# Kernel tuning notes

Measured on AMD Instinct MI355X. Metric: run time of the kernel, lower is better.

## Reference

```python
import jax, jax.numpy as jnp
import numpy as np

NB_NEIGHBORS = 8


def _euclidean_distances(X):
    # X: (n, d); pairwise distances between rows, clamped at 0 before sqrt.
    sq = jnp.sum(jnp.square(X), axis=1)  # (n,)
    d = -2.0 * (X @ X.T) + sq[None, :] + sq[:, None]
    return jnp.sqrt(jnp.maximum(d, 0.0))


def setup_inputs() -> dict:
    key = jax.random.key(0)
    k1, k2 = jax.random.split(key)
    B, C, F, D3 = 64, 4, 8192, 1
    d_coord = 64
    inputs = jax.random.normal(k1, (B, C, F, D3), dtype=jnp.float32)
    coordinates = jax.random.normal(k2, (d_coord, 1, F), dtype=jnp.float32)
    return {"inputs": inputs, "coordinates": coordinates}


def reference(inputs, coordinates):
    # coordinates: (d, 1, F) -> crd: (d, F); features are columns.
    d, _, F = coordinates.shape
    crd = coordinates.reshape(d, F)
    dist = _euclidean_distances(crd.T)  # (F, F) distances between features
    # top-k smallest distances per feature (indices of nearest features)
    _, idx = jax.lax.top_k(-dist, NB_NEIGHBORS)  # (F, K)
    # Original loop: first slot hardcoded to feature 0, then idx[0,1:],
    # then idx[f,:] for f >= 1. Flatten into one gather index vector.
    flat_idx = jnp.concatenate(
        [jnp.zeros((1,), dtype=idx.dtype), idx[0, 1:], idx[1:].reshape(-1)]
    )  # (F*K,)
    # Single fused gather along the feature axis: (B, C, F*K, D3)
    return jnp.take(inputs, flat_idx, axis=2)
```

## Files before the change

kernel.cpp:

```cpp
#include <hip/hip_runtime.h>

#define F      8192
#define KD     64
#define NB     8
#define WROWS  32
#define MKEEP  16
#define JQ     4
#define CPR    64
#define NROUND ((F / JQ) / CPR)
#define CAP    96
#define MARGIN 0.25f

typedef unsigned long long u64;
typedef unsigned short ushort_t;
typedef __attribute__((ext_vector_type(8))) _Float16 f16x8;
typedef __attribute__((ext_vector_type(4))) float f32x4;

__device__ __forceinline__ u64 pack64(float d, int j) {
    return ((u64)__float_as_uint(d) << 32) | (unsigned)j;
}

template<int CTRL>
__device__ __forceinline__ u64 dpp_u64(u64 x) {
    unsigned lo = (unsigned)x, hi = (unsigned)(x >> 32);
    lo = (unsigned)__builtin_amdgcn_update_dpp(0, (int)lo, CTRL, 0xF, 0xF, true);
    hi = (unsigned)__builtin_amdgcn_update_dpp(0, (int)hi, CTRL, 0xF, 0xF, true);
    return ((u64)hi << 32) | lo;
}
__device__ __forceinline__ u64 swap_xor1(u64 x) { return dpp_u64<0xB1>(x); }
__device__ __forceinline__ u64 swap_xor2(u64 x) { return dpp_u64<0x4E>(x); }
__device__ __forceinline__ u64 swap_xor4(u64 x, int n) {
    u64 shr = dpp_u64<0x114>(x);
    u64 shl = dpp_u64<0x104>(x);
    return (n & 4) ? shr : shl;
}
__device__ __forceinline__ u64 swap_xor8(u64 x, int n) {
    u64 shr = dpp_u64<0x118>(x);
    u64 shl = dpp_u64<0x108>(x);
    return (n & 8) ? shr : shl;
}
__device__ __forceinline__ u64 swap_mirror(u64 x) { return dpp_u64<0x140>(x); }
__device__ __forceinline__ u64 swz_xor16(u64 x) {
    unsigned lo = (unsigned)__builtin_amdgcn_ds_swizzle((int)(unsigned)x, 0x401F);
    unsigned hi = (unsigned)__builtin_amdgcn_ds_swizzle((int)(x >> 32), 0x401F);
    return ((u64)hi << 32) | lo;
}

#define CEK(x, J, K, SW)                                                      \
    { u64 px = SW; bool wmin = ((n & (J)) == 0) == ((n & (K)) == 0);          \
      x = (wmin == (px < x)) ? px : x; }
#define CEA(L, J, SW)                                                         \
    { u64 pl = SW; bool wmin = ((n & (J)) == 0);                              \
      L = (wmin == (pl < L)) ? pl : L; }
#define SORT16(x)                                                             \
    CEK(x, 1, 2,  swap_xor1(x))                                               \
    CEK(x, 2, 4,  swap_xor2(x))    CEK(x, 1, 4,  swap_xor1(x))                \
    CEK(x, 4, 8,  swap_xor4(x,n))  CEK(x, 2, 8,  swap_xor2(x))                \
    CEK(x, 1, 8,  swap_xor1(x))                                               \
    CEK(x, 8, 16, swap_xor8(x,n))  CEK(x, 4, 16, swap_xor4(x,n))              \
    CEK(x, 2, 16, swap_xor2(x))    CEK(x, 1, 16, swap_xor1(x))
#define MERGECLEAN(x, Y)                                                      \
    { u64 y = (Y); x = (y < x) ? y : x;                                       \
      CEA(x, 8, swap_xor8(x, n))                                              \
      CEA(x, 4, swap_xor4(x, n))                                              \
      CEA(x, 2, swap_xor2(x))                                                 \
      CEA(x, 1, swap_xor1(x)) }

__global__ __launch_bounds__(256) void prep_kernel(const float* __restrict__ crd,
                                                   float* __restrict__ sq,
                                                   ushort_t* __restrict__ XtH,
                                                   float* __restrict__ Xt32) {
    const int f = blockIdx.x * 256 + threadIdx.x;
    float acc = 0.f;
#pragma unroll
    for (int kb = 0; kb < 8; ++kb) {
        ushort_t hb[8];
        float    xv[8];
#pragma unroll
        for (int u = 0; u < 8; ++u) {
            int k = kb * 8 + u;
            float x = crd[k * F + f];
            acc = fmaf(x, x, acc);
            hb[u] = __builtin_bit_cast(ushort_t, (_Float16)x);
            xv[u] = x;
        }
        *(uint4*)&XtH[(size_t)f * KD + kb * 8] = *(const uint4*)hb;
        *(float4*)&Xt32[(size_t)f * KD + kb * 8]     = *(const float4*)&xv[0];
        *(float4*)&Xt32[(size_t)f * KD + kb * 8 + 4] = *(const float4*)&xv[4];
    }
    sq[f] = acc;
}

__global__ __launch_bounds__(256, 4) void knn_mfma(const ushort_t* __restrict__ XtH,
                                                   const float* __restrict__ sq,
                                                   u64* __restrict__ part) {
    __shared__ u64 buf[WROWS][CAP + 1];
    __shared__ u64 lst[WROWS][MKEEP + 1];
    __shared__ __align__(16) float thr[WROWS];
    __shared__ int cnt[WROWS];

    const int tid  = threadIdx.x;
    const int wave = tid >> 6;
    const int tx   = tid & 63;
    const int quad = tx >> 4;
    const int n    = tx & 15;
    const int blockRow = (blockIdx.x >> 2) * WROWS;
    const int jq    = blockIdx.x & 3;
    const int jbase = jq * (F / JQ);

    if (tid < WROWS) { cnt[tid] = 0; thr[tid] = __int_as_float(0x7f800000); }
#pragma unroll
    for (int e = tid; e < WROWS * MKEEP; e += 256) lst[e >> 4][e & 15] = ~0ULL;
    __syncthreads();

    const size_t a0 = (size_t)(blockRow + n) * KD + quad * 8;
    const size_t a1 = (size_t)(blockRow + 16 + n) * KD + quad * 8;
    const f16x8 a0h0 = *(const f16x8*)(XtH + a0), a0h1 = *(const f16x8*)(XtH + a0 + 32);
    const f16x8 a1h0 = *(const f16x8*)(XtH + a1), a1h1 = *(const f16x8*)(XtH + a1 + 32);
    const f32x4 sqi0 = *(const f32x4*)&sq[blockRow + quad * 4];
    const f32x4 sqi1 = *(const f32x4*)&sq[blockRow + 16 + quad * 4];
    f32x4 pre0, pre1;
#pragma unroll
    for (int r = 0; r < 4; ++r) { pre0[r] = -__int_as_float(0x7f800000);
                                  pre1[r] = -__int_as_float(0x7f800000); }

    const int laneCol = wave * 16 + n;

#define LOADB(H0, H1, SJ, RND)                                                \
    {   int jc = jbase + (RND) * CPR + laneCol;                               \
        size_t bo = (size_t)jc * KD + quad * 8;                               \
        H0 = *(const f16x8*)(XtH + bo); H1 = *(const f16x8*)(XtH + bo + 32);  \
        SJ = sq[jc]; }

#define MFMABODY(H0, H1)                                                      \
        f32x4 za0 = {0,0,0,0}, za1 = {0,0,0,0};                               \
        za0 = __builtin_amdgcn_mfma_f32_16x16x32_f16(a0h0, H0, za0, 0, 0, 0); \
        za0 = __builtin_amdgcn_mfma_f32_16x16x32_f16(a0h1, H1, za0, 0, 0, 0); \
        za1 = __builtin_amdgcn_mfma_f32_16x16x32_f16(a1h0, H0, za1, 0, 0, 0); \
        za1 = __builtin_amdgcn_mfma_f32_16x16x32_f16(a1h1, H1, za1, 0, 0, 0);

#define PROCESS0(H0, H1, SJ, RND)                                             \
    {   MFMABODY(H0, H1)                                                      \
        const int jc = jbase + (RND) * CPR + laneCol;                         \
        _Pragma("unroll")                                                     \
        for (int r = 0; r < 4; ++r) {                                         \
            float d0 = fmaxf((sqi0[r] + SJ) - 2.f * za0[r], 0.f);             \
            buf[quad * 4 + r][laneCol] = pack64(d0, jc);                      \
            float d1 = fmaxf((sqi1[r] + SJ) - 2.f * za1[r], 0.f);             \
            buf[16 + quad * 4 + r][laneCol] = pack64(d1, jc);                 \
        } }

#define PROCESS(H0, H1, SJ, RND)                                              \
    {   MFMABODY(H0, H1)                                                      \
        const int jc = jbase + (RND) * CPR + laneCol;                         \
        const float h = 0.5f * SJ;                                            \
        _Pragma("unroll")                                                     \
        for (int r = 0; r < 4; ++r) {                                         \
            float dot = za0[r];                                               \
            if (dot >= pre0[r] + h) {                                         \
                float d = fmaxf((sqi0[r] + SJ) - 2.f * dot, 0.f);             \
                int row = quad * 4 + r;                                       \
                int q = atomicAdd(&cnt[row], 1);                              \
                if (q < CAP) buf[row][q] = pack64(d, jc);                     \
            }                                                                 \
            dot = za1[r];                                                     \
            if (dot >= pre1[r] + h) {                                         \
                float d = fmaxf((sqi1[r] + SJ) - 2.f * dot, 0.f);             \
                int row = 16 + quad * 4 + r;                                  \
                int q = atomicAdd(&cnt[row], 1);                              \
                if (q < CAP) buf[row][q] = pack64(d, jc);                     \
            }                                                                 \
        } }

#define FOLD(R0)                                                              \
    {   __syncthreads();                                                      \
        _Pragma("unroll")                                                     \
        for (int p = 0; p < 2; ++p) {                                         \
            const int row = p * 16 + wave * 4 + quad;                         \
            u64 Lv = lst[row][n];                                             \
            const u64 tmax = __shfl(Lv, (tx & 48) | 15, 64);                  \
            const int nn = (R0) ? CPR : min(cnt[row], CAP);                   \
            for (int ii = 0; ii < nn; ii += 16) {                             \
                u64 x = (ii + n < nn) ? buf[row][ii + n] : ~0ULL;             \
                u64 bal = __ballot(x < tmax);                                 \
                if ((unsigned short)(bal >> (quad * 16)) == 0) continue;      \
                SORT16(x)                                                     \
                MERGECLEAN(Lv, swap_mirror(x))                                \
            }                                                                 \
            lst[row][n] = Lv;                                                 \
            if (n == NB - 1) thr[row] = __uint_as_float((unsigned)(Lv >> 32)) + MARGIN; \
            if (n == 0) cnt[row] = 0;                                         \
        }                                                                     \
        __syncthreads();                                                      \
        {   f32x4 t0 = *(const f32x4*)&thr[quad * 4];                         \
            f32x4 t1 = *(const f32x4*)&thr[16 + quad * 4];                    \
            _Pragma("unroll")                                                 \
            for (int r = 0; r < 4; ++r) {                                     \
                pre0[r] = 0.5f * (sqi0[r] - t0[r]);                           \
                pre1[r] = 0.5f * (sqi1[r] - t1[r]);                           \
            } } }

    f16x8 B0h0, B0h1, B1h0, B1h1;
    float B0sj, B1sj;
    LOADB(B0h0, B0h1, B0sj, 0)
    LOADB(B1h0, B1h1, B1sj, 1)

    PROCESS0(B0h0, B0h1, B0sj, 0)
    LOADB(B0h0, B0h1, B0sj, 2)
    FOLD(1)
    PROCESS(B1h0, B1h1, B1sj, 1)
    LOADB(B1h0, B1h1, B1sj, 3)
    FOLD(0)

    for (int rr = 2; rr < NROUND; rr += 2) {
        PROCESS(B0h0, B0h1, B0sj, rr)
        if (rr + 2 < NROUND) LOADB(B0h0, B0h1, B0sj, rr + 2)
        PROCESS(B1h0, B1h1, B1sj, rr + 1)
        if (rr + 3 < NROUND) LOADB(B1h0, B1h1, B1sj, rr + 3)
        if (((rr + 1) & (rr + 2)) == 0) FOLD(0)
    }

#pragma unroll
    for (int e = tid; e < WROWS * MKEEP; e += 256) {
        int rrw = e >> 4, ss = e & 15;
        part[((size_t)jq * F + blockRow + rrw) * MKEEP + ss] = lst[rrw][ss];
    }
#undef LOADB
#undef MFMABODY
#undef PROCESS0
#undef PROCESS
#undef FOLD
}

__global__ __launch_bounds__(256) void recheck_kernel(const float* __restrict__ Xt32,
                                                      const float* __restrict__ sq,
                                                      const u64* __restrict__ part,
                                                      int* __restrict__ knn) {
    __shared__ float A_s[4][KD];
    const int tid = threadIdx.x;
    const int rl = tid >> 6, tx = tid & 63;
    const int n  = tx & 15;
    const int i = blockIdx.x * 4 + rl;

    A_s[tid >> 6][tid & 63] = Xt32[(size_t)(blockIdx.x * 4 + (tid >> 6)) * KD + (tid & 63)];
    __syncthreads();

    u64 pc = part[((size_t)(tx >> 4) * F + i) * MKEEP + (tx & 15)];
    int j = (int)(pc & 0xffffffffu);

    const float4* b4 = (const float4*)(Xt32 + (size_t)j * KD);
    float acc = 0.f;
#pragma unroll
    for (int kk = 0; kk < KD / 4; ++kk) {
        float4 b = b4[kk];
        const float* a = &A_s[rl][kk * 4];
        acc = fmaf(a[0], b.x, acc);
        acc = fmaf(a[1], b.y, acc);
        acc = fmaf(a[2], b.z, acc);
        acc = fmaf(a[3], b.w, acc);
    }
    float d = fmaxf((sq[i] + sq[j]) - 2.f * acc, 0.f);
    u64 x = pack64(d, j);

    SORT16(x)
    MERGECLEAN(x, swz_xor16(swap_mirror(x)))
    MERGECLEAN(x, __shfl_xor(swap_mirror(x), 32, 64))

    if (tx < NB) knn[(size_t)i * NB + tx] = (int)(x & 0xffffffffu);
}

__global__ __launch_bounds__(512) void gather_kernel(const float* __restrict__ inp,
                                                     const int* __restrict__ knn,
                                                     float* __restrict__ out) {
    __shared__ float row[F];
    const int bc    = blockIdx.x >> 2;
    const int chunk = blockIdx.x & 3;
    const int tid   = threadIdx.x;

    const float4* in4  = (const float4*)(inp + (size_t)bc * F);
    float4*       row4 = (float4*)row;
#pragma unroll
    for (int i = 0; i < (F / 4) / 512; ++i) row4[i * 512 + tid] = in4[i * 512 + tid];
    __syncthreads();

    const int4* kn4 = (const int4*)knn;
    float4*     ou4 = (float4*)(out + (size_t)bc * (F * NB));

#pragma unroll
    for (int i = 0; i < 8; ++i) {
        int e = chunk * 4096 + i * 512 + tid;
        int4 idx = kn4[e];
        if (e == 0) idx.x = 0;
        float4 o;
        o.x = row[idx.x]; o.y = row[idx.y]; o.z = row[idx.z]; o.w = row[idx.w];
        ou4[e] = o;
    }
}

extern "C" void kernel_launch(void* const* d_in, const int* in_sizes, int n_in,
                              void* d_out, int out_size, void* d_ws, size_t ws_size,
                              hipStream_t stream) {
    const float* inp = (const float*)d_in[0];
    const float* crd = (const float*)d_in[1];
    float* out = (float*)d_out;

    ushort_t* XtH  = (ushort_t*)d_ws;
    float*    Xt32 = (float*)((char*)d_ws + (2u << 20));
    float*    sq   = (float*)((char*)d_ws + (4u << 20));
    int*      knn  = (int*)((char*)d_ws + (4u << 20) + (1u << 15));
    u64*      part = (u64*)((char*)d_ws + (5u << 20));

    prep_kernel<<<F / 256, 256, 0, stream>>>(crd, sq, XtH, Xt32);
    knn_mfma<<<(F / WROWS) * JQ, 256, 0, stream>>>(XtH, sq, part);
    recheck_kernel<<<F / 4, 256, 0, stream>>>(Xt32, sq, part, knn);
    gather_kernel<<<256 * 4, 512, 0, stream>>>(inp, knn, out);
}
```

Baseline: 163.2 us.

## Fuse four kernels into one persistent kernel with software grid barriers

Merges the prep, kNN MFMA, recheck and gather kernels into one 1024-block kernel whose phases are separated by atomic-counter grid barriers, with a shared-memory union reused across phases. The aim is to remove the per-launch gaps and tail drain between the four launches. In exchange it adds barrier spin and atomic traffic and relies on all 1024 blocks being resident at once, which the launch bounds suggest but do not guarantee. The gather phase now runs with 256 threads per block instead of 512, and a memset is added before each launch to reset the barrier counters.

```diff
diff --git a/kernel.cpp b/kernel.cpp
--- a/kernel.cpp
+++ b/kernel.cpp
@@ -10,6 +10,7 @@
 #define NROUND ((F / JQ) / CPR)
 #define CAP    96
 #define MARGIN 0.25f
+#define GRID   1024
 
 typedef unsigned long long u64;
 typedef unsigned short ushort_t;
@@ -18,6 +19,21 @@
 
 __device__ __forceinline__ u64 pack64(float d, int j) {
     return ((u64)__float_as_uint(d) << 32) | (unsigned)j;
+}
+
+__device__ __forceinline__ void gbar(unsigned* cnt, unsigned* rel) {
+    __syncthreads();
+    if (threadIdx.x == 0) {
+        __threadfence();
+        unsigned v = atomicAdd(cnt, 1u);
+        if (v == GRID - 1) {
+            atomicExch(rel, 1u);
+        } else {
+            while (atomicAdd(rel, 0u) == 0u) __builtin_amdgcn_s_sleep(8);
+        }
+        __threadfence();
+    }
+    __syncthreads();
 }
 
 template<int CTRL>
@@ -66,65 +82,75 @@
       CEA(x, 2, swap_xor2(x))                                                 \
       CEA(x, 1, swap_xor1(x)) }
 
-__global__ __launch_bounds__(256) void prep_kernel(const float* __restrict__ crd,
-                                                   float* __restrict__ sq,
-                                                   ushort_t* __restrict__ XtH,
-                                                   float* __restrict__ Xt32) {
-    const int f = blockIdx.x * 256 + threadIdx.x;
-    float acc = 0.f;
-#pragma unroll
-    for (int kb = 0; kb < 8; ++kb) {
-        ushort_t hb[8];
-        float    xv[8];
-#pragma unroll
-        for (int u = 0; u < 8; ++u) {
-            int k = kb * 8 + u;
-            float x = crd[k * F + f];
-            acc = fmaf(x, x, acc);
-            hb[u] = __builtin_bit_cast(ushort_t, (_Float16)x);
-            xv[u] = x;
-        }
-        *(uint4*)&XtH[(size_t)f * KD + kb * 8] = *(const uint4*)hb;
-        *(float4*)&Xt32[(size_t)f * KD + kb * 8]     = *(const float4*)&xv[0];
-        *(float4*)&Xt32[(size_t)f * KD + kb * 8 + 4] = *(const float4*)&xv[4];
-    }
-    sq[f] = acc;
-}
-
-__global__ __launch_bounds__(256, 4) void knn_mfma(const ushort_t* __restrict__ XtH,
-                                                   const float* __restrict__ sq,
-                                                   u64* __restrict__ part) {
-    __shared__ u64 buf[WROWS][CAP + 1];
-    __shared__ u64 lst[WROWS][MKEEP + 1];
-    __shared__ __align__(16) float thr[WROWS];
-    __shared__ int cnt[WROWS];
-
+__global__ __launch_bounds__(256, 4) void fused_kernel(
+        const float* __restrict__ inp, const float* __restrict__ crd,
+        float* __restrict__ out, ushort_t* __restrict__ XtH,
+        float* __restrict__ Xt32, float* __restrict__ sq,
+        int* __restrict__ knn, u64* __restrict__ part,
+        unsigned* __restrict__ bar) {
+    __shared__ union ShMem {
+        struct {
+            u64 buf[WROWS][CAP + 1];
+            u64 lst[WROWS][MKEEP + 1];
+            float thr[WROWS];
+            int cnt[WROWS];
+        } k;
+        float row[F];
+        float A_s[4][KD];
+    } sh;
+
+    const int bid  = blockIdx.x;
     const int tid  = threadIdx.x;
     const int wave = tid >> 6;
     const int tx   = tid & 63;
     const int quad = tx >> 4;
     const int n    = tx & 15;
-    const int blockRow = (blockIdx.x >> 2) * WROWS;
-    const int jq    = blockIdx.x & 3;
-    const int jbase = jq * (F / JQ);
-
-    if (tid < WROWS) { cnt[tid] = 0; thr[tid] = __int_as_float(0x7f800000); }
-#pragma unroll
-    for (int e = tid; e < WROWS * MKEEP; e += 256) lst[e >> 4][e & 15] = ~0ULL;
-    __syncthreads();
-
-    const size_t a0 = (size_t)(blockRow + n) * KD + quad * 8;
-    const size_t a1 = (size_t)(blockRow + 16 + n) * KD + quad * 8;
-    const f16x8 a0h0 = *(const f16x8*)(XtH + a0), a0h1 = *(const f16x8*)(XtH + a0 + 32);
-    const f16x8 a1h0 = *(const f16x8*)(XtH + a1), a1h1 = *(const f16x8*)(XtH + a1 + 32);
-    const f32x4 sqi0 = *(const f32x4*)&sq[blockRow + quad * 4];
-    const f32x4 sqi1 = *(const f32x4*)&sq[blockRow + 16 + quad * 4];
-    f32x4 pre0, pre1;
-#pragma unroll
-    for (int r = 0; r < 4; ++r) { pre0[r] = -__int_as_float(0x7f800000);
-                                  pre1[r] = -__int_as_float(0x7f800000); }
-
-    const int laneCol = wave * 16 + n;
+
+    if (bid < F / 256) {
+        const int f = bid * 256 + tid;
+        float acc = 0.f;
+#pragma unroll
+        for (int kb = 0; kb < 8; ++kb) {
+            ushort_t hb[8];
+            float    xv[8];
+#pragma unroll
+            for (int u = 0; u < 8; ++u) {
+                int k = kb * 8 + u;
+                float x = crd[k * F + f];
+                acc = fmaf(x, x, acc);
+                hb[u] = __builtin_bit_cast(ushort_t, (_Float16)x);
+                xv[u] = x;
+            }
+            *(uint4*)&XtH[(size_t)f * KD + kb * 8] = *(const uint4*)hb;
+            *(float4*)&Xt32[(size_t)f * KD + kb * 8]     = *(const float4*)&xv[0];
+            *(float4*)&Xt32[(size_t)f * KD + kb * 8 + 4] = *(const float4*)&xv[4];
+        }
+        sq[f] = acc;
+    }
+    gbar(&bar[0], &bar[1]);
+
+    {
+        const int blockRow = (bid >> 2) * WROWS;
+        const int jq    = bid & 3;
+        const int jbase = jq * (F / JQ);
+
+        if (tid < WROWS) { sh.k.cnt[tid] = 0; sh.k.thr[tid] = __int_as_float(0x7f800000); }
+#pragma unroll
+        for (int e = tid; e < WROWS * MKEEP; e += 256) sh.k.lst[e >> 4][e & 15] = ~0ULL;
+        __syncthreads();
+
+        const size_t a0 = (size_t)(blockRow + n) * KD + quad * 8;
+        const size_t a1 = (size_t)(blockRow + 16 + n) * KD + quad * 8;
+        const f16x8 a0h0 = *(const f16x8*)(XtH + a0), a0h1 = *(const f16x8*)(XtH + a0 + 32);
+        const f16x8 a1h0 = *(const f16x8*)(XtH + a1), a1h1 = *(const f16x8*)(XtH + a1 + 32);
+        const f32x4 sqi0 = *(const f32x4*)&sq[blockRow + quad * 4];
+        const f32x4 sqi1 = *(const f32x4*)&sq[blockRow + 16 + quad * 4];
+        f32x4 pre0, pre1;
+#pragma unroll
+        for (int r = 0; r < 4; ++r) { pre0[r] = -__int_as_float(0x7f800000);
+                                      pre1[r] = -__int_as_float(0x7f800000); }
+
+        const int laneCol = wave * 16 + n;
 
 #define LOADB(H0, H1, SJ, RND)                                                \
     {   int jc = jbase + (RND) * CPR + laneCol;                               \
@@ -145,9 +171,9 @@
         _Pragma("unroll")                                                     \
         for (int r = 0; r < 4; ++r) {                                         \
             float d0 = fmaxf((sqi0[r] + SJ) - 2.f * za0[r], 0.f);             \
-            buf[quad * 4 + r][laneCol] = pack64(d0, jc);                      \
+            sh.k.buf[quad * 4 + r][laneCol] = pack64(d0, jc);                 \
             float d1 = fmaxf((sqi1[r] + SJ) - 2.f * za1[r], 0.f);             \
-            buf[16 + quad * 4 + r][laneCol] = pack64(d1, jc);                 \
+            sh.k.buf[16 + quad * 4 + r][laneCol] = pack64(d1, jc);            \
         } }
 
 #define PROCESS(H0, H1, SJ, RND)                                              \
@@ -160,15 +186,15 @@
             if (dot >= pre0[r] + h) {                                         \
                 float d = fmaxf((sqi0[r] + SJ) - 2.f * dot, 0.f);             \
                 int row = quad * 4 + r;                                       \
-                int q = atomicAdd(&cnt[row], 1);                              \
-                if (q < CAP) buf[row][q] = pack64(d, jc);                     \
+                int q = atomicAdd(&sh.k.cnt[row], 1);                         \
+                if (q < CAP) sh.k.buf[row][q] = pack64(d, jc);                \
             }                                                                 \
             dot = za1[r];                                                     \
             if (dot >= pre1[r] + h) {                                         \
                 float d = fmaxf((sqi1[r] + SJ) - 2.f * dot, 0.f);             \
                 int row = 16 + quad * 4 + r;                                  \
-                int q = atomicAdd(&cnt[row], 1);                              \
-                if (q < CAP) buf[row][q] = pack64(d, jc);                     \
+                int q = atomicAdd(&sh.k.cnt[row], 1);                         \
+                if (q < CAP) sh.k.buf[row][q] = pack64(d, jc);                \
             }                                                                 \
         } }
 
@@ -177,123 +203,118 @@
         _Pragma("unroll")                                                     \
         for (int p = 0; p < 2; ++p) {                                         \
             const int row = p * 16 + wave * 4 + quad;                         \
-            u64 Lv = lst[row][n];                                             \
+            u64 Lv = sh.k.lst[row][n];                                        \
             const u64 tmax = __shfl(Lv, (tx & 48) | 15, 64);                  \
-            const int nn = (R0) ? CPR : min(cnt[row], CAP);                   \
+            const int nn = (R0) ? CPR : min(sh.k.cnt[row], CAP);              \
             for (int ii = 0; ii < nn; ii += 16) {                             \
-                u64 x = (ii + n < nn) ? buf[row][ii + n] : ~0ULL;             \
+                u64 x = (ii + n < nn) ? sh.k.buf[row][ii + n] : ~0ULL;        \
                 u64 bal = __ballot(x < tmax);                                 \
                 if ((unsigned short)(bal >> (quad * 16)) == 0) continue;      \
                 SORT16(x)                                                     \
                 MERGECLEAN(Lv, swap_mirror(x))                                \
             }                                                                 \
-            lst[row][n] = Lv;                                                 \
-            if (n == NB - 1) thr[row] = __uint_as_float((unsigned)(Lv >> 32)) + MARGIN; \
-            if (n == 0) cnt[row] = 0;                                         \
+            sh.k.lst[row][n] = Lv;                                            \
+            if (n == NB - 1) sh.k.thr[row] = __uint_as_float((unsigned)(Lv >> 32)) + MARGIN; \
+            if (n == 0) sh.k.cnt[row] = 0;                                    \
         }                                                                     \
         __syncthreads();                                                      \
-        {   f32x4 t0 = *(const f32x4*)&thr[quad * 4];                         \
-            f32x4 t1 = *(const f32x4*)&thr[16 + quad * 4];                    \
+        {   f32x4 t0 = *(const f32x4*)&sh.k.thr[quad * 4];                    \
+            f32x4 t1 = *(const f32x4*)&sh.k.thr[16 + quad * 4];               \
             _Pragma("unroll")                                                 \
             for (int r = 0; r < 4; ++r) {                                     \
                 pre0[r] = 0.5f * (sqi0[r] - t0[r]);                           \
                 pre1[r] = 0.5f * (sqi1[r] - t1[r]);                           \
             } } }
 
-    f16x8 B0h0, B0h1, B1h0, B1h1;
-    float B0sj, B1sj;
-    LOADB(B0h0, B0h1, B0sj, 0)
-    LOADB(B1h0, B1h1, B1sj, 1)
-
-    PROCESS0(B0h0, B0h1, B0sj, 0)
-    LOADB(B0h0, B0h1, B0sj, 2)
-    FOLD(1)
-    PROCESS(B1h0, B1h1, B1sj, 1)
-    LOADB(B1h0, B1h1, B1sj, 3)
-    FOLD(0)
-
-    for (int rr = 2; rr < NROUND; rr += 2) {
-        PROCESS(B0h0, B0h1, B0sj, rr)
-        if (rr + 2 < NROUND) LOADB(B0h0, B0h1, B0sj, rr + 2)
-        PROCESS(B1h0, B1h1, B1sj, rr + 1)
-        if (rr + 3 < NROUND) LOADB(B1h0, B1h1, B1sj, rr + 3)
-        if (((rr + 1) & (rr + 2)) == 0) FOLD(0)
-    }
-
-#pragma unroll
-    for (int e = tid; e < WROWS * MKEEP; e += 256) {
-        int rrw = e >> 4, ss = e & 15;
-        part[((size_t)jq * F + blockRow + rrw) * MKEEP + ss] = lst[rrw][ss];
-    }
+        f16x8 B0h0, B0h1, B1h0, B1h1;
+        float B0sj, B1sj;
+        LOADB(B0h0, B0h1, B0sj, 0)
+        LOADB(B1h0, B1h1, B1sj, 1)
+
+        PROCESS0(B0h0, B0h1, B0sj, 0)
+        LOADB(B0h0, B0h1, B0sj, 2)
+        FOLD(1)
+        PROCESS(B1h0, B1h1, B1sj, 1)
+        LOADB(B1h0, B1h1, B1sj, 3)
+        FOLD(0)
+
+        for (int rr = 2; rr < NROUND; rr += 2) {
+            PROCESS(B0h0, B0h1, B0sj, rr)
+            if (rr + 2 < NROUND) LOADB(B0h0, B0h1, B0sj, rr + 2)
+            PROCESS(B1h0, B1h1, B1sj, rr + 1)
+            if (rr + 3 < NROUND) LOADB(B1h0, B1h1, B1sj, rr + 3)
+            if (((rr + 1) & (rr + 2)) == 0) FOLD(0)
+        }
+
+#pragma unroll
+        for (int e = tid; e < WROWS * MKEEP; e += 256) {
+            int rrw = e >> 4, ss = e & 15;
+            part[((size_t)jq * F + blockRow + rrw) * MKEEP + ss] = sh.k.lst[rrw][ss];
+        }
 #undef LOADB
 #undef MFMABODY
 #undef PROCESS0
 #undef PROCESS
 #undef FOLD
-}
-
-__global__ __launch_bounds__(256) void recheck_kernel(const float* __restrict__ Xt32,
-                                                      const float* __restrict__ sq,
-                                                      const u64* __restrict__ part,
-                                                      int* __restrict__ knn) {
-    __shared__ float A_s[4][KD];
-    const int tid = threadIdx.x;
-    const int rl = tid >> 6, tx = tid & 63;
-    const int n  = tx & 15;
-    const int i = blockIdx.x * 4 + rl;
-
-    A_s[tid >> 6][tid & 63] = Xt32[(size_t)(blockIdx.x * 4 + (tid >> 6)) * KD + (tid & 63)];
-    __syncthreads();
-
-    u64 pc = part[((size_t)(tx >> 4) * F + i) * MKEEP + (tx & 15)];
-    int j = (int)(pc & 0xffffffffu);
-
-    const float4* b4 = (const float4*)(Xt32 + (size_t)j * KD);
-    float acc = 0.f;
-#pragma unroll
-    for (int kk = 0; kk < KD / 4; ++kk) {
-        float4 b = b4[kk];
-        const float* a = &A_s[rl][kk * 4];
-        acc = fmaf(a[0], b.x, acc);
-        acc = fmaf(a[1], b.y, acc);
-        acc = fmaf(a[2], b.z, acc);
-        acc = fmaf(a[3], b.w, acc);
-    }
-    float d = fmaxf((sq[i] + sq[j]) - 2.f * acc, 0.f);
-    u64 x = pack64(d, j);
-
-    SORT16(x)
-    MERGECLEAN(x, swz_xor16(swap_mirror(x)))
-    MERGECLEAN(x, __shfl_xor(swap_mirror(x), 32, 64))
-
-    if (tx < NB) knn[(size_t)i * NB + tx] = (int)(x & 0xffffffffu);
-}
-
-__global__ __launch_bounds__(512) void gather_kernel(const float* __restrict__ inp,
-                                                     const int* __restrict__ knn,
-                                                     float* __restrict__ out) {
-    __shared__ float row[F];
-    const int bc    = blockIdx.x >> 2;
-    const int chunk = blockIdx.x & 3;
-    const int tid   = threadIdx.x;
-
-    const float4* in4  = (const float4*)(inp + (size_t)bc * F);
-    float4*       row4 = (float4*)row;
-#pragma unroll
-    for (int i = 0; i < (F / 4) / 512; ++i) row4[i * 512 + tid] = in4[i * 512 + tid];
-    __syncthreads();
-
-    const int4* kn4 = (const int4*)knn;
-    float4*     ou4 = (float4*)(out + (size_t)bc * (F * NB));
-
-#pragma unroll
-    for (int i = 0; i < 8; ++i) {
-        int e = chunk * 4096 + i * 512 + tid;
-        int4 idx = kn4[e];
-        if (e == 0) idx.x = 0;
-        float4 o;
-        o.x = row[idx.x]; o.y = row[idx.y]; o.z = row[idx.z]; o.w = row[idx.w];
-        ou4[e] = o;
+    }
+    gbar(&bar[2], &bar[3]);
+
+    for (int g = bid; g < F / 4; g += GRID) {
+        const int rl = wave;
+        const int i = g * 4 + rl;
+
+        sh.A_s[tid >> 6][tid & 63] = Xt32[(size_t)(g * 4 + (tid >> 6)) * KD + (tid & 63)];
+        __syncthreads();
+
+        u64 pc = part[((size_t)(tx >> 4) * F + i) * MKEEP + (tx & 15)];
+        int j = (int)(pc & 0xffffffffu);
+
+        const float4* b4 = (const float4*)(Xt32 + (size_t)j * KD);
+        float acc = 0.f;
+#pragma unroll
+        for (int kk = 0; kk < KD / 4; ++kk) {
+            float4 b = b4[kk];
+            const float* a = &sh.A_s[rl][kk * 4];
+            acc = fmaf(a[0], b.x, acc);
+            acc = fmaf(a[1], b.y, acc);
+            acc = fmaf(a[2], b.z, acc);
+            acc = fmaf(a[3], b.w, acc);
+        }
+        float d = fmaxf((sq[i] + sq[j]) - 2.f * acc, 0.f);
+        u64 x = pack64(d, j);
+
+        SORT16(x)
+        MERGECLEAN(x, swz_xor16(swap_mirror(x)))
+        MERGECLEAN(x, __shfl_xor(swap_mirror(x), 32, 64))
+
+        if (tx < NB) knn[(size_t)i * NB + tx] = (int)(x & 0xffffffffu);
+        __syncthreads();
+    }
+    gbar(&bar[4], &bar[5]);
+
+    {
+        const int bc    = bid >> 2;
+        const int chunk = bid & 3;
+
+        const float4* in4  = (const float4*)(inp + (size_t)bc * F);
+        float4*       row4 = (float4*)sh.row;
+#pragma unroll
+        for (int i2 = 0; i2 < (F / 4) / 256; ++i2) row4[i2 * 256 + tid] = in4[i2 * 256 + tid];
+        __syncthreads();
+
+        const int4* kn4 = (const int4*)knn;
+        float4*     ou4 = (float4*)(out + (size_t)bc * (F * NB));
+
+#pragma unroll
+        for (int i2 = 0; i2 < 16; ++i2) {
+            int e = chunk * 4096 + i2 * 256 + tid;
+            int4 idx = kn4[e];
+            if (e == 0) idx.x = 0;
+            float4 o;
+            o.x = sh.row[idx.x]; o.y = sh.row[idx.y];
+            o.z = sh.row[idx.z]; o.w = sh.row[idx.w];
+            ou4[e] = o;
+        }
     }
 }
 
@@ -305,13 +326,13 @@
     float* out = (float*)d_out;
 
     ushort_t* XtH  = (ushort_t*)d_ws;
+    unsigned* bar  = (unsigned*)((char*)d_ws + (1u << 20));
     float*    Xt32 = (float*)((char*)d_ws + (2u << 20));
     float*    sq   = (float*)((char*)d_ws + (4u << 20));
     int*      knn  = (int*)((char*)d_ws + (4u << 20) + (1u << 15));
     u64*      part = (u64*)((char*)d_ws + (5u << 20));
 
-    prep_kernel<<<F / 256, 256, 0, stream>>>(crd, sq, XtH, Xt32);
-    knn_mfma<<<(F / WROWS) * JQ, 256, 0, stream>>>(XtH, sq, part);
-    recheck_kernel<<<F / 4, 256, 0, stream>>>(Xt32, sq, part, knn);
-    gather_kernel<<<256 * 4, 512, 0, stream>>>(inp, knn, out);
-}
+    hipMemsetAsync(bar, 0, 64, stream);
+    hipLaunchKernelGGL(fused_kernel, dim3(GRID), dim3(256), 0, stream,
+                       inp, crd, out, XtH, Xt32, sq, knn, part, bar);
+}
```

After: 465.1 us. 2.85x slower.
